# Performance work log

Measured on AMD Instinct MI355X. Metric: run time of the kernel, lower is better.

## Reference

```python
import jax, jax.numpy as jnp
import numpy as np

BOOST_STRENGTH = 1.0  # init kwarg boostStrength (already >= 0)


def setup_inputs() -> dict:
    key = jax.random.key(0)
    k1, k2 = jax.random.split(key)
    x = jax.random.normal(k1, (8192, 4096), dtype=jnp.float32)
    # duty cycles are running fractions of activity, roughly around k/n
    dutyCycles = jax.random.uniform(k2, (4096,), dtype=jnp.float32) * 0.2
    return {"x": x, "dutyCycles": dutyCycles, "k": 409}


def reference(x, dutyCycles, k):
    n = x.shape[1]
    boost_strength = jnp.maximum(jnp.float32(BOOST_STRENGTH), 0.0)
    target_density = jnp.float32(k) / jnp.float32(n)
    # boostFactors = exp[(targetDensity - dutyCycle) * boostStrength]
    boost_factors = jnp.exp((target_density - dutyCycles) * boost_strength)  # [n]
    boosted = x * boost_factors  # [B, n]
    topk_vals, _ = jax.lax.top_k(boosted, k)  # [B, k]
    bottom = jnp.min(topk_vals, axis=1, keepdims=True)  # per-row k-th largest
    mask = (boosted >= bottom).astype(x.dtype)
    return x * mask
```

## Files before the change

### kernel.cpp

```cpp
#include <hip/hip_runtime.h>
#include <cstdint>
#include <cstddef>

#define N_COLS 4096
#define TPB 256
#define WPB 4
#define HSTRW 260
#define SURV_CAP 64

__global__ void boost_kernel(const float* __restrict__ dc,
                             const int* __restrict__ kp,
                             float* __restrict__ bf) {
    int i = blockIdx.x * blockDim.x + threadIdx.x;
    if (i < N_COLS) {
        float td = (float)kp[0] / (float)N_COLS;
        float arg = td - dc[i];
        bf[i] = (float)exp((double)arg);
    }
}

__device__ __forceinline__ uint32_t orderable(uint32_t u) {
    return (u & 0x80000000u) ? ~u : (u | 0x80000000u);
}

__device__ __forceinline__ void wave_lgkm() {
    asm volatile("s_waitcnt lgkmcnt(0)" ::: "memory");
}

__global__ __launch_bounds__(TPB, 4) void kwinner_kernel(
    const float* __restrict__ x, const float* __restrict__ bf,
    const int* __restrict__ kp, float* __restrict__ out, int rows)
{
    __shared__ __align__(16) float    s_bf[N_COLS];
    __shared__ __align__(16) uint32_t s_hist[WPB][2][HSTRW];
    __shared__ uint32_t s_cand[WPB][SURV_CAP];
    __shared__ uint32_t s_m2[WPB * 8];

    const int tid  = threadIdx.x;
    const int w    = tid >> 6;
    const int lane = tid & 63;

    {
        const float4* br = (const float4*)bf;
        float4* sb = (float4*)s_bf;
        #pragma unroll
        for (int j = 0; j < 4; ++j) sb[tid + j * TPB] = br[tid + j * TPB];
    }
    __syncthreads();

    size_t row = (size_t)blockIdx.x * WPB + (size_t)w;
    const size_t rmax = (size_t)rows - 1;
    if (row > rmax) row = rmax;

    const float4* xr   = (const float4*)(x + row * (size_t)N_COLS);
    float4*       orow = (float4*)(out + row * (size_t)N_COLS);
    const float4* bf4  = (const float4*)s_bf;

    float4 xv[16];
    #pragma unroll
    for (int jj = 0; jj < 16; ++jj) xv[jj] = xr[lane + 64 * jj];

    uint32_t* hist = &s_hist[w][0][0];
    uint32_t* m2p  = &s_m2[w * 8];

    {
        uint4 z; z.x = z.y = z.z = z.w = 0u;
        *(uint4*)&hist[4 * lane]         = z;
        *(uint4*)&hist[HSTRW + 4 * lane] = z;
        if (lane == 0) *m2p = 0u;
    }
    wave_lgkm();

    const uint32_t cofs = (uint32_t)(lane & 1) * HSTRW;
    const float T0f = 1.10f;
    #pragma unroll
    for (int jj = 0; jj < 16; ++jj) {
        float4 b = bf4[lane + 64 * jj];
        float xb0 = xv[jj].x * b.x, xb1 = xv[jj].y * b.y;
        float xb2 = xv[jj].z * b.z, xb3 = xv[jj].w * b.w;
        if (xb0 >= T0f) { uint32_t d = (__float_as_uint(xb0) >> 16) - 0x3F80u; d = d > 255u ? 255u : d; atomicAdd(&hist[cofs + d], 1u); }
        if (xb1 >= T0f) { uint32_t d = (__float_as_uint(xb1) >> 16) - 0x3F80u; d = d > 255u ? 255u : d; atomicAdd(&hist[cofs + d], 1u); }
        if (xb2 >= T0f) { uint32_t d = (__float_as_uint(xb2) >> 16) - 0x3F80u; d = d > 255u ? 255u : d; atomicAdd(&hist[cofs + d], 1u); }
        if (xb3 >= T0f) { uint32_t d = (__float_as_uint(xb3) >> 16) - 0x3F80u; d = d > 255u ? 255u : d; atomicAdd(&hist[cofs + d], 1u); }
    }
    wave_lgkm();

    const uint32_t k = (uint32_t)kp[0];
    uint32_t rem = k;

    uint32_t dsel, packed;
    {
        uint4 a  = *(const uint4*)&hist[4 * lane];
        uint4 b2 = *(const uint4*)&hist[HSTRW + 4 * lane];
        uint32_t vv0 = a.x + b2.x, vv1 = a.y + b2.y, vv2 = a.z + b2.z, vv3 = a.w + b2.w;
        uint32_t s3 = vv3, s2 = vv2 + s3, s1 = vv1 + s2, s0 = vv0 + s1;
        uint32_t T = s0;
        #pragma unroll
        for (int off = 1; off < 64; off <<= 1) {
            uint32_t t = (uint32_t)__shfl_down((int)T, off, 64);
            if (lane + off < 64) T += t;
        }
        uint32_t Tex = T - s0;
        uint32_t S0 = Tex + s0, S1 = Tex + s1, S2 = Tex + s2, S3 = Tex + s3;
        int b = -1; uint32_t sn = 0;
        if (S3 >= rem)      { b = 3; sn = S3 - vv3; }
        else if (S2 >= rem) { b = 2; sn = S2 - vv2; }
        else if (S1 >= rem) { b = 1; sn = S1 - vv1; }
        else if (S0 >= rem) { b = 0; sn = S0 - vv0; }
        packed = (b >= 0) ? ((((uint32_t)(4 * lane + b + 1)) << 16) | sn) : 0u;
        #pragma unroll
        for (int off = 1; off < 64; off <<= 1) {
            uint32_t o = (uint32_t)__shfl_xor((int)packed, off, 64);
            packed = packed > o ? packed : o;
        }
        dsel = (packed >> 16) - 1u;
        rem -= (packed & 0xFFFFu);
    }

    float thr = 0.0f;
    bool need_fallback = (packed == 0u) || (dsel == 255u);

    if (!need_fallback) {
        const uint32_t hi16 = 0x3F80u + dsel;
        #pragma unroll
        for (int jj = 0; jj < 16; ++jj) {
            float4 b = bf4[lane + 64 * jj];
            float xb0 = xv[jj].x * b.x, xb1 = xv[jj].y * b.y;
            float xb2 = xv[jj].z * b.z, xb3 = xv[jj].w * b.w;
            uint32_t u0 = __float_as_uint(xb0), u1 = __float_as_uint(xb1);
            uint32_t u2 = __float_as_uint(xb2), u3 = __float_as_uint(xb3);
            if ((u0 >> 16) == hi16) { uint32_t p = atomicAdd(m2p, 1u); if (p < SURV_CAP) s_cand[w][p] = u0; }
            if ((u1 >> 16) == hi16) { uint32_t p = atomicAdd(m2p, 1u); if (p < SURV_CAP) s_cand[w][p] = u1; }
            if ((u2 >> 16) == hi16) { uint32_t p = atomicAdd(m2p, 1u); if (p < SURV_CAP) s_cand[w][p] = u2; }
            if ((u3 >> 16) == hi16) { uint32_t p = atomicAdd(m2p, 1u); if (p < SURV_CAP) s_cand[w][p] = u3; }
        }
        wave_lgkm();
        const uint32_t m2 = *m2p;
        if (m2 <= SURV_CAP) {
            uint32_t cv = ((uint32_t)lane < m2) ? s_cand[w][lane] : ((~hi16) << 16);
            uint32_t cur = 0;
            #pragma unroll
            for (int bpos = 15; bpos >= 0; --bpos) {
                uint32_t t  = (hi16 << 16) | cur | (1u << bpos);
                uint32_t mk = ~((1u << bpos) - 1u);
                uint32_t c  = (uint32_t)__popcll(__ballot(((cv ^ t) & mk) == 0u));
                if (c >= rem) cur |= (1u << bpos);
                else          rem -= c;
            }
            thr = __uint_as_float((hi16 << 16) | cur);
        } else {
            need_fallback = true;
        }
    }

    if (need_fallback) {
        {
            uint4 z; z.x = z.y = z.z = z.w = 0u;
            *(uint4*)&hist[4 * lane]         = z;
            *(uint4*)&hist[HSTRW + 4 * lane] = z;
        }
        wave_lgkm();
        uint32_t prefix = 0;
        rem = k;
        const uint32_t pmasks[4] = {0u, 0xFF000000u, 0xFFFF0000u, 0xFFFFFF00u};
        #pragma unroll 1
        for (int pass = 0; pass < 4; ++pass) {
            const int shift = 24 - pass * 8;
            const uint32_t pm = pmasks[pass];
            #pragma unroll
            for (int jj = 0; jj < 16; ++jj) {
                float4 b = bf4[lane + 64 * jj];
                float xb0 = xv[jj].x * b.x, xb1 = xv[jj].y * b.y;
                float xb2 = xv[jj].z * b.z, xb3 = xv[jj].w * b.w;
                uint32_t ou;
                ou = orderable(__float_as_uint(xb0));
                if (((ou ^ prefix) & pm) == 0u) atomicAdd(&hist[cofs + ((ou >> shift) & 255u)], 1u);
                ou = orderable(__float_as_uint(xb1));
                if (((ou ^ prefix) & pm) == 0u) atomicAdd(&hist[cofs + ((ou >> shift) & 255u)], 1u);
                ou = orderable(__float_as_uint(xb2));
                if (((ou ^ prefix) & pm) == 0u) atomicAdd(&hist[cofs + ((ou >> shift) & 255u)], 1u);
                ou = orderable(__float_as_uint(xb3));
                if (((ou ^ prefix) & pm) == 0u) atomicAdd(&hist[cofs + ((ou >> shift) & 255u)], 1u);
            }
            wave_lgkm();
            uint4 a  = *(const uint4*)&hist[4 * lane];
            uint4 b2 = *(const uint4*)&hist[HSTRW + 4 * lane];
            {
                uint4 z; z.x = z.y = z.z = z.w = 0u;
                *(uint4*)&hist[4 * lane]         = z;
                *(uint4*)&hist[HSTRW + 4 * lane] = z;
            }
            wave_lgkm();
            uint32_t vv0 = a.x + b2.x, vv1 = a.y + b2.y, vv2 = a.z + b2.z, vv3 = a.w + b2.w;
            uint32_t s3 = vv3, s2 = vv2 + s3, s1 = vv1 + s2, s0 = vv0 + s1;
            uint32_t T = s0;
            #pragma unroll
            for (int off = 1; off < 64; off <<= 1) {
                uint32_t t = (uint32_t)__shfl_down((int)T, off, 64);
                if (lane + off < 64) T += t;
            }
            uint32_t Tex = T - s0;
            uint32_t S0 = Tex + s0, S1 = Tex + s1, S2 = Tex + s2, S3 = Tex + s3;
            int b = -1; uint32_t sn = 0;
            if (S3 >= rem)      { b = 3; sn = S3 - vv3; }
            else if (S2 >= rem) { b = 2; sn = S2 - vv2; }
            else if (S1 >= rem) { b = 1; sn = S1 - vv1; }
            else if (S0 >= rem) { b = 0; sn = S0 - vv0; }
            uint32_t pk = (b >= 0) ? ((((uint32_t)(4 * lane + b + 1)) << 16) | sn) : 0u;
            #pragma unroll
            for (int off = 1; off < 64; off <<= 1) {
                uint32_t o = (uint32_t)__shfl_xor((int)pk, off, 64);
                pk = pk > o ? pk : o;
            }
            prefix |= ((pk >> 16) - 1u) << shift;
            rem -= (pk & 0xFFFFu);
        }
        uint32_t tu = (prefix & 0x80000000u) ? (prefix & 0x7FFFFFFFu) : ~prefix;
        thr = __uint_as_float(tu);
    }

    #pragma unroll
    for (int jj = 0; jj < 16; ++jj) {
        float4 b = bf4[lane + 64 * jj];
        float4 o;
        o.x = (xv[jj].x * b.x >= thr) ? xv[jj].x : 0.0f;
        o.y = (xv[jj].y * b.y >= thr) ? xv[jj].y : 0.0f;
        o.z = (xv[jj].z * b.z >= thr) ? xv[jj].z : 0.0f;
        o.w = (xv[jj].w * b.w >= thr) ? xv[jj].w : 0.0f;
        orow[lane + 64 * jj] = o;
    }
}

extern "C" void kernel_launch(void* const* d_in, const int* in_sizes, int n_in,
                              void* d_out, int out_size, void* d_ws, size_t ws_size,
                              hipStream_t stream) {
    const float* x  = (const float*)d_in[0];
    const float* dc = (const float*)d_in[1];
    const int*   kp = (const int*)d_in[2];
    float* out = (float*)d_out;
    float* bf  = (float*)d_ws;

    const int n    = in_sizes[1];
    const int rows = in_sizes[0] / n;

    boost_kernel<<<(n + TPB - 1) / TPB, TPB, 0, stream>>>(dc, kp, bf);
    const int nb = (rows + WPB - 1) / WPB;
    kwinner_kernel<<<nb, TPB, 0, stream>>>(x, bf, kp, out, rows);
}
```

Baseline: 242.9 us.

## Keep boosted values in registers, drop shared boost staging, re-read x for output

Removes the shared-memory copy of boost factors and the block barrier, instead reading boost factors from global (L2-cached) once per element and keeping the boosted products in registers. The x row is re-read from global in the final masking pass instead of being held in registers. Block size is halved to two waves per block. This cuts repeated LDS reads and multiplies in every pass, at the cost of a second global read of x (likely served from cache) and more blocks.

```diff
diff --git a/kernel.cpp b/kernel.cpp
--- a/kernel.cpp
+++ b/kernel.cpp
@@ -3,8 +3,8 @@
 #include <cstddef>
 
 #define N_COLS 4096
-#define TPB 256
-#define WPB 4
+#define TPB 128
+#define WPB 2
 #define HSTRW 260
 #define SURV_CAP 64
 
@@ -31,7 +31,6 @@
     const float* __restrict__ x, const float* __restrict__ bf,
     const int* __restrict__ kp, float* __restrict__ out, int rows)
 {
-    __shared__ __align__(16) float    s_bf[N_COLS];
     __shared__ __align__(16) uint32_t s_hist[WPB][2][HSTRW];
     __shared__ uint32_t s_cand[WPB][SURV_CAP];
     __shared__ uint32_t s_m2[WPB * 8];
@@ -40,25 +39,26 @@
     const int w    = tid >> 6;
     const int lane = tid & 63;
 
-    {
-        const float4* br = (const float4*)bf;
-        float4* sb = (float4*)s_bf;
-        #pragma unroll
-        for (int j = 0; j < 4; ++j) sb[tid + j * TPB] = br[tid + j * TPB];
-    }
-    __syncthreads();
-
     size_t row = (size_t)blockIdx.x * WPB + (size_t)w;
     const size_t rmax = (size_t)rows - 1;
     if (row > rmax) row = rmax;
 
     const float4* xr   = (const float4*)(x + row * (size_t)N_COLS);
     float4*       orow = (float4*)(out + row * (size_t)N_COLS);
-    const float4* bf4  = (const float4*)s_bf;
-
-    float4 xv[16];
-    #pragma unroll
-    for (int jj = 0; jj < 16; ++jj) xv[jj] = xr[lane + 64 * jj];
+    const float4* bf4  = (const float4*)bf;
+
+    float xb[64];
+    #pragma unroll
+    for (int jj = 0; jj < 16; ++jj) {
+        float4 v = xr[lane + 64 * jj];
+        float4 b = bf4[lane + 64 * jj];
+        xb[jj * 4 + 0] = v.x * b.x;
+        xb[jj * 4 + 1] = v.y * b.y;
+        xb[jj * 4 + 2] = v.z * b.z;
+        xb[jj * 4 + 3] = v.w * b.w;
+    }
+    #pragma unroll
+    for (int e = 0; e < 64; ++e) asm volatile("" : "+v"(xb[e]));
 
     uint32_t* hist = &s_hist[w][0][0];
     uint32_t* m2p  = &s_m2[w * 8];
@@ -74,14 +74,12 @@
     const uint32_t cofs = (uint32_t)(lane & 1) * HSTRW;
     const float T0f = 1.10f;
     #pragma unroll
-    for (int jj = 0; jj < 16; ++jj) {
-        float4 b = bf4[lane + 64 * jj];
-        float xb0 = xv[jj].x * b.x, xb1 = xv[jj].y * b.y;
-        float xb2 = xv[jj].z * b.z, xb3 = xv[jj].w * b.w;
-        if (xb0 >= T0f) { uint32_t d = (__float_as_uint(xb0) >> 16) - 0x3F80u; d = d > 255u ? 255u : d; atomicAdd(&hist[cofs + d], 1u); }
-        if (xb1 >= T0f) { uint32_t d = (__float_as_uint(xb1) >> 16) - 0x3F80u; d = d > 255u ? 255u : d; atomicAdd(&hist[cofs + d], 1u); }
-        if (xb2 >= T0f) { uint32_t d = (__float_as_uint(xb2) >> 16) - 0x3F80u; d = d > 255u ? 255u : d; atomicAdd(&hist[cofs + d], 1u); }
-        if (xb3 >= T0f) { uint32_t d = (__float_as_uint(xb3) >> 16) - 0x3F80u; d = d > 255u ? 255u : d; atomicAdd(&hist[cofs + d], 1u); }
+    for (int e = 0; e < 64; ++e) {
+        if (xb[e] >= T0f) {
+            uint32_t d = (__float_as_uint(xb[e]) >> 16) - 0x3F80u;
+            d = d > 255u ? 255u : d;
+            atomicAdd(&hist[cofs + d], 1u);
+        }
     }
     wave_lgkm();
 
@@ -123,16 +121,12 @@
     if (!need_fallback) {
         const uint32_t hi16 = 0x3F80u + dsel;
         #pragma unroll
-        for (int jj = 0; jj < 16; ++jj) {
-            float4 b = bf4[lane + 64 * jj];
-            float xb0 = xv[jj].x * b.x, xb1 = xv[jj].y * b.y;
-            float xb2 = xv[jj].z * b.z, xb3 = xv[jj].w * b.w;
-            uint32_t u0 = __float_as_uint(xb0), u1 = __float_as_uint(xb1);
-            uint32_t u2 = __float_as_uint(xb2), u3 = __float_as_uint(xb3);
-            if ((u0 >> 16) == hi16) { uint32_t p = atomicAdd(m2p, 1u); if (p < SURV_CAP) s_cand[w][p] = u0; }
-            if ((u1 >> 16) == hi16) { uint32_t p = atomicAdd(m2p, 1u); if (p < SURV_CAP) s_cand[w][p] = u1; }
-            if ((u2 >> 16) == hi16) { uint32_t p = atomicAdd(m2p, 1u); if (p < SURV_CAP) s_cand[w][p] = u2; }
-            if ((u3 >> 16) == hi16) { uint32_t p = atomicAdd(m2p, 1u); if (p < SURV_CAP) s_cand[w][p] = u3; }
+        for (int e = 0; e < 64; ++e) {
+            uint32_t ub = __float_as_uint(xb[e]);
+            if ((ub >> 16) == hi16) {
+                uint32_t p = atomicAdd(m2p, 1u);
+                if (p < SURV_CAP) s_cand[w][p] = ub;
+            }
         }
         wave_lgkm();
         const uint32_t m2 = *m2p;
@@ -168,19 +162,10 @@
             const int shift = 24 - pass * 8;
             const uint32_t pm = pmasks[pass];
             #pragma unroll
-            for (int jj = 0; jj < 16; ++jj) {
-                float4 b = bf4[lane + 64 * jj];
-                float xb0 = xv[jj].x * b.x, xb1 = xv[jj].y * b.y;
-                float xb2 = xv[jj].z * b.z, xb3 = xv[jj].w * b.w;
-                uint32_t ou;
-                ou = orderable(__float_as_uint(xb0));
-                if (((ou ^ prefix) & pm) == 0u) atomicAdd(&hist[cofs + ((ou >> shift) & 255u)], 1u);
-                ou = orderable(__float_as_uint(xb1));
-                if (((ou ^ prefix) & pm) == 0u) atomicAdd(&hist[cofs + ((ou >> shift) & 255u)], 1u);
-                ou = orderable(__float_as_uint(xb2));
-                if (((ou ^ prefix) & pm) == 0u) atomicAdd(&hist[cofs + ((ou >> shift) & 255u)], 1u);
-                ou = orderable(__float_as_uint(xb3));
-                if (((ou ^ prefix) & pm) == 0u) atomicAdd(&hist[cofs + ((ou >> shift) & 255u)], 1u);
+            for (int e = 0; e < 64; ++e) {
+                uint32_t ou = orderable(__float_as_uint(xb[e]));
+                if (((ou ^ prefix) & pm) == 0u)
+                    atomicAdd(&hist[cofs + ((ou >> shift) & 255u)], 1u);
             }
             wave_lgkm();
             uint4 a  = *(const uint4*)&hist[4 * lane];
@@ -221,12 +206,12 @@
 
     #pragma unroll
     for (int jj = 0; jj < 16; ++jj) {
-        float4 b = bf4[lane + 64 * jj];
+        float4 v = xr[lane + 64 * jj];
         float4 o;
-        o.x = (xv[jj].x * b.x >= thr) ? xv[jj].x : 0.0f;
-        o.y = (xv[jj].y * b.y >= thr) ? xv[jj].y : 0.0f;
-        o.z = (xv[jj].z * b.z >= thr) ? xv[jj].z : 0.0f;
-        o.w = (xv[jj].w * b.w >= thr) ? xv[jj].w : 0.0f;
+        o.x = (xb[jj * 4 + 0] >= thr) ? v.x : 0.0f;
+        o.y = (xb[jj * 4 + 1] >= thr) ? v.y : 0.0f;
+        o.z = (xb[jj * 4 + 2] >= thr) ? v.z : 0.0f;
+        o.w = (xb[jj * 4 + 3] >= thr) ? v.w : 0.0f;
         orow[lane + 64 * jj] = o;
     }
 }
```

Result: slower. 320.6 us (+32.0%).

## Drop register row cache and LDS boost copy; re-read from global for occupancy

Applied to the files above, without the earlier changes.

Each wave no longer keeps its whole 4096-float row in 64 VGPRs, and the block no longer stages the boost factors into 16 KB of LDS. Every pass (histogram, candidate gather, fallback passes, final mask) now re-reads x and the boost factors from global memory, relying on the cache. This frees registers and LDS, and launch bounds are raised to 8 blocks per CU for more occupancy. The trade is two to three times more global and L2 traffic per row, plus a possible cache miss on the row re-reads in a kernel that is already memory bound.

```diff
diff --git a/kernel.cpp b/kernel.cpp
--- a/kernel.cpp
+++ b/kernel.cpp
@@ -5,7 +5,7 @@
 #define N_COLS 4096
 #define TPB 256
 #define WPB 4
-#define HSTRW 260
+#define CSTR 260
 #define SURV_CAP 64
 
 __global__ void boost_kernel(const float* __restrict__ dc,
@@ -27,12 +27,11 @@
     asm volatile("s_waitcnt lgkmcnt(0)" ::: "memory");
 }
 
-__global__ __launch_bounds__(TPB, 4) void kwinner_kernel(
+__global__ __launch_bounds__(TPB, 8) void kwinner_kernel(
     const float* __restrict__ x, const float* __restrict__ bf,
     const int* __restrict__ kp, float* __restrict__ out, int rows)
 {
-    __shared__ __align__(16) float    s_bf[N_COLS];
-    __shared__ __align__(16) uint32_t s_hist[WPB][2][HSTRW];
+    __shared__ __align__(16) uint32_t s_hist[WPB][2][CSTR];
     __shared__ uint32_t s_cand[WPB][SURV_CAP];
     __shared__ uint32_t s_m2[WPB * 8];
 
@@ -40,48 +39,36 @@
     const int w    = tid >> 6;
     const int lane = tid & 63;
 
-    {
-        const float4* br = (const float4*)bf;
-        float4* sb = (float4*)s_bf;
-        #pragma unroll
-        for (int j = 0; j < 4; ++j) sb[tid + j * TPB] = br[tid + j * TPB];
-    }
-    __syncthreads();
-
     size_t row = (size_t)blockIdx.x * WPB + (size_t)w;
     const size_t rmax = (size_t)rows - 1;
     if (row > rmax) row = rmax;
 
     const float4* xr   = (const float4*)(x + row * (size_t)N_COLS);
     float4*       orow = (float4*)(out + row * (size_t)N_COLS);
-    const float4* bf4  = (const float4*)s_bf;
-
-    float4 xv[16];
-    #pragma unroll
-    for (int jj = 0; jj < 16; ++jj) xv[jj] = xr[lane + 64 * jj];
+    const float4* bfr  = (const float4*)bf;
 
     uint32_t* hist = &s_hist[w][0][0];
     uint32_t* m2p  = &s_m2[w * 8];
 
     {
         uint4 z; z.x = z.y = z.z = z.w = 0u;
-        *(uint4*)&hist[4 * lane]         = z;
-        *(uint4*)&hist[HSTRW + 4 * lane] = z;
+        *(uint4*)&hist[4 * lane]        = z;
+        *(uint4*)&hist[CSTR + 4 * lane] = z;
         if (lane == 0) *m2p = 0u;
     }
     wave_lgkm();
 
-    const uint32_t cofs = (uint32_t)(lane & 1) * HSTRW;
+    const uint32_t cofs = (uint32_t)(lane & 1) * CSTR;
     const float T0f = 1.10f;
     #pragma unroll
     for (int jj = 0; jj < 16; ++jj) {
-        float4 b = bf4[lane + 64 * jj];
-        float xb0 = xv[jj].x * b.x, xb1 = xv[jj].y * b.y;
-        float xb2 = xv[jj].z * b.z, xb3 = xv[jj].w * b.w;
-        if (xb0 >= T0f) { uint32_t d = (__float_as_uint(xb0) >> 16) - 0x3F80u; d = d > 255u ? 255u : d; atomicAdd(&hist[cofs + d], 1u); }
-        if (xb1 >= T0f) { uint32_t d = (__float_as_uint(xb1) >> 16) - 0x3F80u; d = d > 255u ? 255u : d; atomicAdd(&hist[cofs + d], 1u); }
-        if (xb2 >= T0f) { uint32_t d = (__float_as_uint(xb2) >> 16) - 0x3F80u; d = d > 255u ? 255u : d; atomicAdd(&hist[cofs + d], 1u); }
-        if (xb3 >= T0f) { uint32_t d = (__float_as_uint(xb3) >> 16) - 0x3F80u; d = d > 255u ? 255u : d; atomicAdd(&hist[cofs + d], 1u); }
+        float4 v = xr[lane + 64 * jj];
+        float4 b = bfr[lane + 64 * jj];
+        float p0 = v.x * b.x, p1 = v.y * b.y, p2 = v.z * b.z, p3 = v.w * b.w;
+        if (p0 >= T0f) { uint32_t d = (__float_as_uint(p0) >> 16) - 0x3F80u; d = d > 255u ? 255u : d; atomicAdd(&hist[cofs + d], 1u); }
+        if (p1 >= T0f) { uint32_t d = (__float_as_uint(p1) >> 16) - 0x3F80u; d = d > 255u ? 255u : d; atomicAdd(&hist[cofs + d], 1u); }
+        if (p2 >= T0f) { uint32_t d = (__float_as_uint(p2) >> 16) - 0x3F80u; d = d > 255u ? 255u : d; atomicAdd(&hist[cofs + d], 1u); }
+        if (p3 >= T0f) { uint32_t d = (__float_as_uint(p3) >> 16) - 0x3F80u; d = d > 255u ? 255u : d; atomicAdd(&hist[cofs + d], 1u); }
     }
     wave_lgkm();
 
@@ -91,7 +78,7 @@
     uint32_t dsel, packed;
     {
         uint4 a  = *(const uint4*)&hist[4 * lane];
-        uint4 b2 = *(const uint4*)&hist[HSTRW + 4 * lane];
+        uint4 b2 = *(const uint4*)&hist[CSTR + 4 * lane];
         uint32_t vv0 = a.x + b2.x, vv1 = a.y + b2.y, vv2 = a.z + b2.z, vv3 = a.w + b2.w;
         uint32_t s3 = vv3, s2 = vv2 + s3, s1 = vv1 + s2, s0 = vv0 + s1;
         uint32_t T = s0;
@@ -124,11 +111,10 @@
         const uint32_t hi16 = 0x3F80u + dsel;
         #pragma unroll
         for (int jj = 0; jj < 16; ++jj) {
-            float4 b = bf4[lane + 64 * jj];
-            float xb0 = xv[jj].x * b.x, xb1 = xv[jj].y * b.y;
-            float xb2 = xv[jj].z * b.z, xb3 = xv[jj].w * b.w;
-            uint32_t u0 = __float_as_uint(xb0), u1 = __float_as_uint(xb1);
-            uint32_t u2 = __float_as_uint(xb2), u3 = __float_as_uint(xb3);
+            float4 v = xr[lane + 64 * jj];
+            float4 b = bfr[lane + 64 * jj];
+            uint32_t u0 = __float_as_uint(v.x * b.x), u1 = __float_as_uint(v.y * b.y);
+            uint32_t u2 = __float_as_uint(v.z * b.z), u3 = __float_as_uint(v.w * b.w);
             if ((u0 >> 16) == hi16) { uint32_t p = atomicAdd(m2p, 1u); if (p < SURV_CAP) s_cand[w][p] = u0; }
             if ((u1 >> 16) == hi16) { uint32_t p = atomicAdd(m2p, 1u); if (p < SURV_CAP) s_cand[w][p] = u1; }
             if ((u2 >> 16) == hi16) { uint32_t p = atomicAdd(m2p, 1u); if (p < SURV_CAP) s_cand[w][p] = u2; }
@@ -156,8 +142,8 @@
     if (need_fallback) {
         {
             uint4 z; z.x = z.y = z.z = z.w = 0u;
-            *(uint4*)&hist[4 * lane]         = z;
-            *(uint4*)&hist[HSTRW + 4 * lane] = z;
+            *(uint4*)&hist[4 * lane]        = z;
+            *(uint4*)&hist[CSTR + 4 * lane] = z;
         }
         wave_lgkm();
         uint32_t prefix = 0;
@@ -169,26 +155,25 @@
             const uint32_t pm = pmasks[pass];
             #pragma unroll
             for (int jj = 0; jj < 16; ++jj) {
-                float4 b = bf4[lane + 64 * jj];
-                float xb0 = xv[jj].x * b.x, xb1 = xv[jj].y * b.y;
-                float xb2 = xv[jj].z * b.z, xb3 = xv[jj].w * b.w;
+                float4 v = xr[lane + 64 * jj];
+                float4 b = bfr[lane + 64 * jj];
                 uint32_t ou;
-                ou = orderable(__float_as_uint(xb0));
-                if (((ou ^ prefix) & pm) == 0u) atomicAdd(&hist[cofs + ((ou >> shift) & 255u)], 1u);
-                ou = orderable(__float_as_uint(xb1));
-                if (((ou ^ prefix) & pm) == 0u) atomicAdd(&hist[cofs + ((ou >> shift) & 255u)], 1u);
-                ou = orderable(__float_as_uint(xb2));
-                if (((ou ^ prefix) & pm) == 0u) atomicAdd(&hist[cofs + ((ou >> shift) & 255u)], 1u);
-                ou = orderable(__float_as_uint(xb3));
+                ou = orderable(__float_as_uint(v.x * b.x));
+                if (((ou ^ prefix) & pm) == 0u) atomicAdd(&hist[cofs + ((ou >> shift) & 255u)], 1u);
+                ou = orderable(__float_as_uint(v.y * b.y));
+                if (((ou ^ prefix) & pm) == 0u) atomicAdd(&hist[cofs + ((ou >> shift) & 255u)], 1u);
+                ou = orderable(__float_as_uint(v.z * b.z));
+                if (((ou ^ prefix) & pm) == 0u) atomicAdd(&hist[cofs + ((ou >> shift) & 255u)], 1u);
+                ou = orderable(__float_as_uint(v.w * b.w));
                 if (((ou ^ prefix) & pm) == 0u) atomicAdd(&hist[cofs + ((ou >> shift) & 255u)], 1u);
             }
             wave_lgkm();
             uint4 a  = *(const uint4*)&hist[4 * lane];
-            uint4 b2 = *(const uint4*)&hist[HSTRW + 4 * lane];
+            uint4 b2 = *(const uint4*)&hist[CSTR + 4 * lane];
             {
                 uint4 z; z.x = z.y = z.z = z.w = 0u;
-                *(uint4*)&hist[4 * lane]         = z;
-                *(uint4*)&hist[HSTRW + 4 * lane] = z;
+                *(uint4*)&hist[4 * lane]        = z;
+                *(uint4*)&hist[CSTR + 4 * lane] = z;
             }
             wave_lgkm();
             uint32_t vv0 = a.x + b2.x, vv1 = a.y + b2.y, vv2 = a.z + b2.z, vv3 = a.w + b2.w;
@@ -221,12 +206,13 @@
 
     #pragma unroll
     for (int jj = 0; jj < 16; ++jj) {
-        float4 b = bf4[lane + 64 * jj];
+        float4 v = xr[lane + 64 * jj];
+        float4 b = bfr[lane + 64 * jj];
         float4 o;
-        o.x = (xv[jj].x * b.x >= thr) ? xv[jj].x : 0.0f;
-        o.y = (xv[jj].y * b.y >= thr) ? xv[jj].y : 0.0f;
-        o.z = (xv[jj].z * b.z >= thr) ? xv[jj].z : 0.0f;
-        o.w = (xv[jj].w * b.w >= thr) ? xv[jj].w : 0.0f;
+        o.x = (v.x * b.x >= thr) ? v.x : 0.0f;
+        o.y = (v.y * b.y >= thr) ? v.y : 0.0f;
+        o.z = (v.z * b.z >= thr) ? v.z : 0.0f;
+        o.w = (v.w * b.w >= thr) ? v.w : 0.0f;
         orow[lane + 64 * jj] = o;
     }
 }
```

Result: slower. 363.6 us (+49.7%).
